# Kernel optimization log

Measured on AMD Instinct MI355X. Metric: run time of the kernel, lower is better.

Reference implementation:

```python
import jax, jax.numpy as jnp
import numpy as np

B, NF, V, D, NI = 16384, 26, 100000, 16, 13
HID = [512, 256, 128, 64, 1]

def setup_inputs() -> dict:
    key = jax.random.key(0)
    ks = jax.random.split(key, 24)
    x_int = jax.random.normal(ks[0], (B, NI), dtype=jnp.float32)
    x_cat = jax.random.randint(ks[1], (B, NF), 0, V, dtype=jnp.int64)
    emb_tables = jax.random.normal(ks[2], (NF, V, D), dtype=jnp.float32) * 0.01
    lin_tables = jax.random.normal(ks[3], (NF, V, 1), dtype=jnp.float32) * 0.01
    W_num = jax.random.normal(ks[4], (NI, 1), dtype=jnp.float32) * 0.1
    b_num = jnp.zeros((1,), dtype=jnp.float32)
    bias = jnp.zeros((1,), dtype=jnp.float32)
    dims = [NF * D + NI] + HID  # 429 -> 512 -> 256 -> 128 -> 64 -> 1
    mlp = {}
    for li in range(5):
        fan_in = dims[li]
        mlp[f'W{li+1}'] = jax.random.normal(ks[5 + 2*li], (dims[li], dims[li+1]), dtype=jnp.float32) / np.sqrt(fan_in)
        mlp[f'b{li+1}'] = jnp.zeros((dims[li+1],), dtype=jnp.float32)
    return dict(x_int=x_int, x_cat=x_cat, emb_tables=emb_tables, lin_tables=lin_tables,
                W_num=W_num, b_num=b_num, bias=bias, **mlp)

def reference(x_int, x_cat, emb_tables, lin_tables, W_num, b_num, bias,
              W1, b1, W2, b2, W3, b3, W4, b4, W5, b5):
    feat_idx = jnp.arange(NF)[None, :]                 # [1, NF]
    emb = emb_tables[feat_idx, x_cat]                  # [B, NF, D] fused gather
    # FM second-order interaction
    sum_emb = jnp.sum(emb, axis=1)                     # [B, D]
    square_of_sum = sum_emb ** 2
    sum_of_square = jnp.sum(emb ** 2, axis=1)
    fm_score = 0.5 * jnp.sum(square_of_sum - sum_of_square, axis=1, keepdims=True)  # [B,1]
    # linear terms
    lin_cat_score = jnp.sum(lin_tables[feat_idx, x_cat], axis=1)  # [B,1]
    lin_num_score = x_int @ W_num + b_num                          # [B,1]
    # deep MLP (dropout is identity at inference)
    deep_in = jnp.concatenate([emb.reshape(emb.shape[0], -1), x_int], axis=1)  # [B, NF*D+NI]
    h = jax.nn.relu(deep_in @ W1 + b1)
    h = jax.nn.relu(h @ W2 + b2)
    h = jax.nn.relu(h @ W3 + b3)
    h = jax.nn.relu(h @ W4 + b4)
    deep_score = h @ W5 + b5                                       # [B,1]
    return bias + lin_cat_score + lin_num_score + fm_score + deep_score
```

## Files before the change

kernel.cpp:

```cpp
#include <hip/hip_runtime.h>
#include <hip/hip_bf16.h>
#include <stdint.h>

typedef __bf16 bf16x8 __attribute__((ext_vector_type(8)));
typedef __bf16 bf16x4 __attribute__((ext_vector_type(4)));
typedef float  f32x4  __attribute__((ext_vector_type(4)));

#define NROWS 16384
#define NFEAT 26
#define VOCAB 100000

__device__ __forceinline__ void bar_lgkm() {
  asm volatile("s_waitcnt lgkmcnt(0)" ::: "memory");
  __builtin_amdgcn_s_barrier();
  asm volatile("" ::: "memory");
}

template<int KPAD, int KREAL, int N, int NCT, int WS>
__device__ __forceinline__ void mlp_layer(const float* __restrict__ W,
                                          const float* __restrict__ bias,
                                          const __bf16* Ain, __bf16* Aout,
                                          int w, int lane) {
  constexpr int LDA = KPAD + 8, LDO = N + 8;
  const int lrow = lane & 15;
  const int kg = (lane >> 4) * 8;

  f32x4 acc[NCT][4];
  #pragma unroll
  for (int j = 0; j < NCT; ++j)
    #pragma unroll
    for (int m = 0; m < 4; ++m)
      #pragma unroll
      for (int i = 0; i < 4; ++i) acc[j][m][i] = 0.f;

  int col[NCT];
  #pragma unroll
  for (int j = 0; j < NCT; ++j) col[j] = (w + j * WS) * 16 + lrow;

  for (int k0 = 0; k0 < KREAL; k0 += 32) {
    bf16x8 af[4];
    #pragma unroll
    for (int m = 0; m < 4; ++m)
      af[m] = *(const bf16x8*)(Ain + (m * 16 + lrow) * LDA + k0 + kg);
    #pragma unroll
    for (int j = 0; j < NCT; ++j) {
      bf16x8 bw;
      #pragma unroll
      for (int i = 0; i < 8; ++i)
        bw[i] = (__bf16)W[(size_t)(k0 + kg + i) * N + col[j]];
      #pragma unroll
      for (int m = 0; m < 4; ++m)
        acc[j][m] = __builtin_amdgcn_mfma_f32_16x16x32_bf16(af[m], bw, acc[j][m], 0, 0, 0);
    }
  }

  const int rbase = (lane >> 4) * 4;
  #pragma unroll
  for (int j = 0; j < NCT; ++j) {
    float bv = bias[col[j]];
    #pragma unroll
    for (int m = 0; m < 4; ++m)
      #pragma unroll
      for (int i = 0; i < 4; ++i) {
        float v = acc[j][m][i] + bv;
        v = fmaxf(v, 0.f);
        Aout[(m * 16 + rbase + i) * LDO + col[j]] = (__bf16)v;
      }
  }
}

__global__ __launch_bounds__(1024) void k_fused(
    const float* __restrict__ x_int,
    const int*   __restrict__ x_cat,
    const float* __restrict__ emb,
    const float* __restrict__ lin,
    const float* __restrict__ W_num,
    const float* __restrict__ b_num,
    const float* __restrict__ bias0,
    const float* __restrict__ W1, const float* __restrict__ b1,
    const float* __restrict__ W2, const float* __restrict__ b2,
    const float* __restrict__ W3, const float* __restrict__ b3,
    const float* __restrict__ W4, const float* __restrict__ b4,
    const float* __restrict__ W5, const float* __restrict__ b5,
    float* __restrict__ out) {
  __shared__ __align__(16) char smem[125184];
  __bf16* A0 = (__bf16*)smem;
  __bf16* A1 = (__bf16*)(smem + 58368);
  int* s_idx = (int*)(smem + 58368);
  float* s_part = (float*)(smem + 124928);

  const int t = threadIdx.x;
  const int row0 = blockIdx.x * 64;
  const int w = t >> 6, lane = t & 63;
  const int lrow = lane & 15, kg = (lane >> 4) * 8;

  for (int i = t; i < 64 * NFEAT; i += 1024) {
    int r = i / NFEAT, f = i - r * NFEAT;
    s_idx[i] = x_cat[(size_t)(row0 + r) * NFEAT + f];
  }
  __syncthreads();

  const int r = t >> 4, d = t & 15;
  const int g = d >> 2, q = d & 3;

  float lin_s = 0.f;
  if (d < 13) {
    lin_s = lin[(size_t)d * VOCAB + s_idx[r * NFEAT + d]]
          + lin[(size_t)(d + 13) * VOCAB + s_idx[r * NFEAT + d + 13]]
          + x_int[(size_t)(row0 + r) * 13 + d] * W_num[d];
  }
  float xv[4] = {0.f, 0.f, 0.f, 0.f};
  if (d >= 8 && d < 12) {
    int base = (d - 8) * 4;
    #pragma unroll
    for (int i = 0; i < 4; ++i)
      if (base + i < 13) xv[i] = x_int[(size_t)(row0 + r) * 13 + base + i];
  }

  f32x4 pf[7];
  #pragma unroll
  for (int c = 0; c < 7; ++c) {
    int fc = 4 * c + g;
    if (fc < NFEAT) {
      int idx = s_idx[r * NFEAT + fc];
      pf[c] = *(const f32x4*)(emb + ((size_t)fc * VOCAB + idx) * 16 + q * 4);
    }
  }

  f32x4 acc[2][4];
  #pragma unroll
  for (int j = 0; j < 2; ++j)
    #pragma unroll
    for (int m = 0; m < 4; ++m)
      #pragma unroll
      for (int i = 0; i < 4; ++i) acc[j][m][i] = 0.f;
  const int colL1[2] = { w * 16 + lrow, (w + 16) * 16 + lrow };

  float fsum[4] = {0.f,0.f,0.f,0.f}, fsq[4] = {0.f,0.f,0.f,0.f};
  #pragma unroll
  for (int c = 0; c < 7; ++c) {
    const int colbase = c * 64 + g * 16 + q * 4;
    if (4 * c + g < NFEAT) {
      bf16x4 pk;
      #pragma unroll
      for (int i = 0; i < 4; ++i) {
        fsum[i] += pf[c][i]; fsq[i] += pf[c][i] * pf[c][i];
        pk[i] = (__bf16)pf[c][i];
      }
      *(bf16x4*)(A0 + r * 456 + colbase) = pk;
    } else {
      bf16x4 pk;
      #pragma unroll
      for (int i = 0; i < 4; ++i) pk[i] = (__bf16)xv[i];
      *(bf16x4*)(A0 + r * 456 + colbase) = pk;
    }
    bar_lgkm();
    #pragma unroll
    for (int ks = 0; ks < 2; ++ks) {
      const int k0 = c * 64 + ks * 32;
      bf16x8 af[4];
      #pragma unroll
      for (int m = 0; m < 4; ++m)
        af[m] = *(const bf16x8*)(A0 + (m * 16 + lrow) * 456 + k0 + kg);
      #pragma unroll
      for (int j = 0; j < 2; ++j) {
        bf16x8 bw;
        #pragma unroll
        for (int i = 0; i < 8; ++i) {
          int k = k0 + kg + i;
          float v;
          if (c < 6) v = W1[(size_t)k * 512 + colL1[j]];
          else       v = (k < 429) ? W1[(size_t)k * 512 + colL1[j]] : 0.f;
          bw[i] = (__bf16)v;
        }
        #pragma unroll
        for (int m = 0; m < 4; ++m)
          acc[j][m] = __builtin_amdgcn_mfma_f32_16x16x32_bf16(af[m], bw, acc[j][m], 0, 0, 0);
      }
    }
  }

  {
    const int rbase = (lane >> 4) * 4;
    #pragma unroll
    for (int j = 0; j < 2; ++j) {
      float bv = b1[colL1[j]];
      #pragma unroll
      for (int m = 0; m < 4; ++m)
        #pragma unroll
        for (int i = 0; i < 4; ++i) {
          float v = acc[j][m][i] + bv;
          v = fmaxf(v, 0.f);
          A1[(m * 16 + rbase + i) * 520 + colL1[j]] = (__bf16)v;
        }
    }
  }

  {
    #pragma unroll
    for (int i = 0; i < 4; ++i) {
      fsum[i] += __shfl_xor(fsum[i], 4); fsq[i] += __shfl_xor(fsq[i], 4);
      fsum[i] += __shfl_xor(fsum[i], 8); fsq[i] += __shfl_xor(fsq[i], 8);
    }
    float fmq = 0.f;
    #pragma unroll
    for (int i = 0; i < 4; ++i) fmq += fsum[i] * fsum[i] - fsq[i];
    fmq += __shfl_xor(fmq, 1);
    fmq += __shfl_xor(fmq, 2);
    float linred = lin_s;
    #pragma unroll
    for (int off = 1; off < 16; off <<= 1) linred += __shfl_xor(linred, off, 16);
    if (d == 0) s_part[r] = 0.5f * fmq + linred + bias0[0] + b_num[0];
  }
  __syncthreads();

  mlp_layer<512, 512, 256, 1, 16>(W2, b2, A1, A0, w, lane);
  __syncthreads();
  if (w < 8) mlp_layer<256, 256, 128, 1, 8>(W3, b3, A0, A1, w, lane);
  __syncthreads();
  if (w < 4) mlp_layer<128, 128, 64, 1, 4>(W4, b4, A1, A0, w, lane);
  __syncthreads();

  {
    const int rr = t >> 4, gg = t & 15;
    float s = 0.f;
    #pragma unroll
    for (int i = 0; i < 4; ++i)
      s += (float)A0[rr * 72 + gg * 4 + i] * W5[gg * 4 + i];
    #pragma unroll
    for (int off = 1; off < 16; off <<= 1) s += __shfl_xor(s, off, 16);
    if (gg == 0) out[row0 + rr] = s + b5[0] + s_part[rr];
  }
}

extern "C" void kernel_launch(void* const* d_in, const int* in_sizes, int n_in,
                              void* d_out, int out_size, void* d_ws, size_t ws_size,
                              hipStream_t stream) {
  const float* x_int = (const float*)d_in[0];
  const int*   x_cat = (const int*)d_in[1];
  const float* emb   = (const float*)d_in[2];
  const float* lin   = (const float*)d_in[3];
  const float* W_num = (const float*)d_in[4];
  const float* b_num = (const float*)d_in[5];
  const float* bias  = (const float*)d_in[6];
  const float* W1 = (const float*)d_in[7];  const float* b1 = (const float*)d_in[8];
  const float* W2 = (const float*)d_in[9];  const float* b2 = (const float*)d_in[10];
  const float* W3 = (const float*)d_in[11]; const float* b3 = (const float*)d_in[12];
  const float* W4 = (const float*)d_in[13]; const float* b4 = (const float*)d_in[14];
  const float* W5 = (const float*)d_in[15]; const float* b5 = (const float*)d_in[16];
  float* out = (float*)d_out;

  k_fused<<<NROWS / 64, 1024, 0, stream>>>(x_int, x_cat, emb, lin, W_num, b_num, bias,
                                           W1, b1, W2, b2, W3, b3, W4, b4, W5, b5,
                                           out);
}
```

Before: 49.66 us.

## Warp-specialize layer 1: producer warps gather embeddings, consumer warps run MFMA

Splits the 16 waves into 8 producer waves and 8 consumer waves. The producers gather embedding rows with a two-chunk-ahead software pipeline and write bf16 activations into shared memory. The consumers run the first-layer MFMAs over four column tiles each, staying in step with the producers through per-chunk barriers. The aim is to overlap the latency of the random embedding gather with the tensor-core work. The cost is that only half the waves issue MFMAs, and each consumer wave holds more accumulator registers.

```diff
diff --git a/kernel.cpp b/kernel.cpp
--- a/kernel.cpp
+++ b/kernel.cpp
@@ -68,6 +68,32 @@
       }
   }
 }
+
+#define P_ISSUE(c)                                                            \
+  if ((c) < 6 || a == 0) {                                                    \
+    int f_ = 4 * (c) + 2 * a;                                                 \
+    int i0_ = s_idx[sbase + f_], i1_ = s_idx[sbase + f_ + 1];                 \
+    pe[(c)][0] = *(const f32x4*)(emb + ((size_t)f_ * VOCAB + i0_) * 16 + q4); \
+    pe[(c)][1] = *(const f32x4*)(emb + ((size_t)(f_ + 1) * VOCAB + i1_) * 16 + q4); \
+  }
+
+#define P_CONSUME(c)                                                          \
+  if ((c) < 6 || a == 0) {                                                    \
+    int f_ = 4 * (c) + 2 * a;                                                 \
+    bf16x4 pk0, pk1;                                                          \
+    for (int i = 0; i < 4; ++i) {                                             \
+      float v0 = pe[(c)][0][i], v1 = pe[(c)][1][i];                           \
+      fsum[i] += v0 + v1; fsq[i] += v0 * v0 + v1 * v1;                        \
+      pk0[i] = (__bf16)v0; pk1[i] = (__bf16)v1;                               \
+    }                                                                         \
+    *(bf16x4*)(A0 + pr * 456 + f_ * 16 + q4) = pk0;                           \
+    *(bf16x4*)(A0 + pr * 456 + (f_ + 1) * 16 + q4) = pk1;                     \
+  } else {                                                                    \
+    bf16x4 pk, pz;                                                            \
+    for (int i = 0; i < 4; ++i) { pk[i] = (__bf16)txv[i]; pz[i] = (__bf16)0.f; } \
+    *(bf16x4*)(A0 + pr * 456 + 416 + q4) = pk;                                \
+    *(bf16x4*)(A0 + pr * 456 + 432 + q4) = pz;                                \
+  }
 
 __global__ __launch_bounds__(1024) void k_fused(
     const float* __restrict__ x_int,
@@ -100,117 +126,106 @@
   }
   __syncthreads();
 
-  const int r = t >> 4, d = t & 15;
-  const int g = d >> 2, q = d & 3;
-
-  float lin_s = 0.f;
-  if (d < 13) {
-    lin_s = lin[(size_t)d * VOCAB + s_idx[r * NFEAT + d]]
-          + lin[(size_t)(d + 13) * VOCAB + s_idx[r * NFEAT + d + 13]]
-          + x_int[(size_t)(row0 + r) * 13 + d] * W_num[d];
-  }
-  float xv[4] = {0.f, 0.f, 0.f, 0.f};
-  if (d >= 8 && d < 12) {
-    int base = (d - 8) * 4;
-    #pragma unroll
-    for (int i = 0; i < 4; ++i)
-      if (base + i < 13) xv[i] = x_int[(size_t)(row0 + r) * 13 + base + i];
-  }
-
-  f32x4 pf[7];
-  #pragma unroll
-  for (int c = 0; c < 7; ++c) {
-    int fc = 4 * c + g;
-    if (fc < NFEAT) {
-      int idx = s_idx[r * NFEAT + fc];
-      pf[c] = *(const f32x4*)(emb + ((size_t)fc * VOCAB + idx) * 16 + q * 4);
-    }
-  }
-
-  f32x4 acc[2][4];
-  #pragma unroll
-  for (int j = 0; j < 2; ++j)
-    #pragma unroll
-    for (int m = 0; m < 4; ++m)
-      #pragma unroll
-      for (int i = 0; i < 4; ++i) acc[j][m][i] = 0.f;
-  const int colL1[2] = { w * 16 + lrow, (w + 16) * 16 + lrow };
-
-  float fsum[4] = {0.f,0.f,0.f,0.f}, fsq[4] = {0.f,0.f,0.f,0.f};
-  #pragma unroll
-  for (int c = 0; c < 7; ++c) {
-    const int colbase = c * 64 + g * 16 + q * 4;
-    if (4 * c + g < NFEAT) {
-      bf16x4 pk;
+  if (w < 8) {
+    const int pid = t;
+    const int pr = pid >> 3;
+    const int sub = pid & 7, a = sub >> 2, q4 = (sub & 3) * 4;
+    const int sbase = pr * NFEAT;
+
+    float lin_acc = lin[(size_t)sub * VOCAB + s_idx[sbase + sub]]
+                  + lin[(size_t)(sub + 8) * VOCAB + s_idx[sbase + sub + 8]]
+                  + lin[(size_t)(sub + 16) * VOCAB + s_idx[sbase + sub + 16]];
+    if (sub < 2)
+      lin_acc += lin[(size_t)(sub + 24) * VOCAB + s_idx[sbase + sub + 24]];
+    float lnum = x_int[(size_t)(row0 + pr) * 13 + sub] * W_num[sub];
+    if (sub < 5)
+      lnum += x_int[(size_t)(row0 + pr) * 13 + sub + 8] * W_num[sub + 8];
+    float txv[4] = {0.f, 0.f, 0.f, 0.f};
+    if (a == 1) {
       #pragma unroll
       for (int i = 0; i < 4; ++i) {
-        fsum[i] += pf[c][i]; fsq[i] += pf[c][i] * pf[c][i];
-        pk[i] = (__bf16)pf[c][i];
+        int ii = q4 + i;
+        if (ii < 13) txv[i] = x_int[(size_t)(row0 + pr) * 13 + ii];
       }
-      *(bf16x4*)(A0 + r * 456 + colbase) = pk;
-    } else {
-      bf16x4 pk;
-      #pragma unroll
-      for (int i = 0; i < 4; ++i) pk[i] = (__bf16)xv[i];
-      *(bf16x4*)(A0 + r * 456 + colbase) = pk;
-    }
-    bar_lgkm();
-    #pragma unroll
-    for (int ks = 0; ks < 2; ++ks) {
-      const int k0 = c * 64 + ks * 32;
-      bf16x8 af[4];
+    }
+
+    float fsum[4] = {0.f,0.f,0.f,0.f}, fsq[4] = {0.f,0.f,0.f,0.f};
+    f32x4 pe[7][2];
+    P_ISSUE(0); P_ISSUE(1);
+    P_ISSUE(2); P_CONSUME(0); bar_lgkm();
+    P_ISSUE(3); P_CONSUME(1); bar_lgkm();
+    P_ISSUE(4); P_CONSUME(2); bar_lgkm();
+    P_ISSUE(5); P_CONSUME(3); bar_lgkm();
+    P_ISSUE(6); P_CONSUME(4); bar_lgkm();
+    P_CONSUME(5); bar_lgkm();
+    P_CONSUME(6); bar_lgkm();
+
+    #pragma unroll
+    for (int i = 0; i < 4; ++i) {
+      fsum[i] += __shfl_xor(fsum[i], 4);
+      fsq[i]  += __shfl_xor(fsq[i], 4);
+    }
+    float fmq = 0.f;
+    #pragma unroll
+    for (int i = 0; i < 4; ++i) fmq += fsum[i] * fsum[i] - fsq[i];
+    fmq += __shfl_xor(fmq, 1);
+    fmq += __shfl_xor(fmq, 2);
+    float lt = lin_acc + lnum;
+    lt += __shfl_xor(lt, 1); lt += __shfl_xor(lt, 2); lt += __shfl_xor(lt, 4);
+    if (sub == 0) s_part[pr] = 0.5f * fmq + lt + bias0[0] + b_num[0];
+  } else {
+    const int cw = w - 8;
+    f32x4 acc[4][4];
+    #pragma unroll
+    for (int j = 0; j < 4; ++j)
       #pragma unroll
       for (int m = 0; m < 4; ++m)
-        af[m] = *(const bf16x8*)(A0 + (m * 16 + lrow) * 456 + k0 + kg);
-      #pragma unroll
-      for (int j = 0; j < 2; ++j) {
-        bf16x8 bw;
-        #pragma unroll
-        for (int i = 0; i < 8; ++i) {
-          int k = k0 + kg + i;
-          float v;
-          if (c < 6) v = W1[(size_t)k * 512 + colL1[j]];
-          else       v = (k < 429) ? W1[(size_t)k * 512 + colL1[j]] : 0.f;
-          bw[i] = (__bf16)v;
+        #pragma unroll
+        for (int i = 0; i < 4; ++i) acc[j][m][i] = 0.f;
+    int col[4];
+    #pragma unroll
+    for (int j = 0; j < 4; ++j) col[j] = (cw + j * 8) * 16 + lrow;
+
+    #pragma unroll
+    for (int c = 0; c < 7; ++c) {
+      bar_lgkm();
+      #pragma unroll
+      for (int ks = 0; ks < 2; ++ks) {
+        const int k0 = c * 64 + ks * 32;
+        bf16x8 af[4];
+        #pragma unroll
+        for (int m = 0; m < 4; ++m)
+          af[m] = *(const bf16x8*)(A0 + (m * 16 + lrow) * 456 + k0 + kg);
+        #pragma unroll
+        for (int j = 0; j < 4; ++j) {
+          bf16x8 bw;
+          #pragma unroll
+          for (int i = 0; i < 8; ++i) {
+            int k = k0 + kg + i;
+            float v;
+            if (c < 6) v = W1[(size_t)k * 512 + col[j]];
+            else       v = (k < 429) ? W1[(size_t)k * 512 + col[j]] : 0.f;
+            bw[i] = (__bf16)v;
+          }
+          #pragma unroll
+          for (int m = 0; m < 4; ++m)
+            acc[j][m] = __builtin_amdgcn_mfma_f32_16x16x32_bf16(af[m], bw, acc[j][m], 0, 0, 0);
         }
-        #pragma unroll
-        for (int m = 0; m < 4; ++m)
-          acc[j][m] = __builtin_amdgcn_mfma_f32_16x16x32_bf16(af[m], bw, acc[j][m], 0, 0, 0);
       }
     }
-  }
-
-  {
     const int rbase = (lane >> 4) * 4;
     #pragma unroll
-    for (int j = 0; j < 2; ++j) {
-      float bv = b1[colL1[j]];
+    for (int j = 0; j < 4; ++j) {
+      float bv = b1[col[j]];
       #pragma unroll
       for (int m = 0; m < 4; ++m)
         #pragma unroll
         for (int i = 0; i < 4; ++i) {
           float v = acc[j][m][i] + bv;
           v = fmaxf(v, 0.f);
-          A1[(m * 16 + rbase + i) * 520 + colL1[j]] = (__bf16)v;
+          A1[(m * 16 + rbase + i) * 520 + col[j]] = (__bf16)v;
         }
     }
-  }
-
-  {
-    #pragma unroll
-    for (int i = 0; i < 4; ++i) {
-      fsum[i] += __shfl_xor(fsum[i], 4); fsq[i] += __shfl_xor(fsq[i], 4);
-      fsum[i] += __shfl_xor(fsum[i], 8); fsq[i] += __shfl_xor(fsq[i], 8);
-    }
-    float fmq = 0.f;
-    #pragma unroll
-    for (int i = 0; i < 4; ++i) fmq += fsum[i] * fsum[i] - fsq[i];
-    fmq += __shfl_xor(fmq, 1);
-    fmq += __shfl_xor(fmq, 2);
-    float linred = lin_s;
-    #pragma unroll
-    for (int off = 1; off < 16; off <<= 1) linred += __shfl_xor(linred, off, 16);
-    if (d == 0) s_part[r] = 0.5f * fmq + linred + bias0[0] + b_num[0];
   }
   __syncthreads();
 
```

New measurement: 73.10 us. 47.2% more time.

## Software-pipeline W1 weight loads and embedding gathers in layer-1 loop

Applied to the files above, without the earlier changes.

Restructures the first MLP layer loop into 14 K-steps, with W1 weight fragments prefetched two steps ahead into a double-buffered register array. Embedding gathers are issued three chunks ahead through a rotating 4-entry buffer instead of all up front. The goal is to overlap global-memory latency for weights and gathered embeddings with the MFMA work. It raises register pressure at 1024 threads per block, which could cause spills.

```diff
diff --git a/kernel.cpp b/kernel.cpp
--- a/kernel.cpp
+++ b/kernel.cpp
@@ -103,6 +103,25 @@
   const int r = t >> 4, d = t & 15;
   const int g = d >> 2, q = d & 3;
 
+  const int colL1[2] = { w * 16 + lrow, (w + 16) * 16 + lrow };
+
+  float wbuf[2][2][8];
+  #pragma unroll
+  for (int sb = 0; sb < 2; ++sb)
+    #pragma unroll
+    for (int j = 0; j < 2; ++j)
+      #pragma unroll
+      for (int i = 0; i < 8; ++i)
+        wbuf[sb][j][i] = W1[(size_t)(sb * 32 + kg + i) * 512 + colL1[j]];
+
+  f32x4 pe[4];
+  #pragma unroll
+  for (int c = 0; c < 3; ++c) {
+    int fc = 4 * c + g;
+    int idx = s_idx[r * NFEAT + fc];
+    pe[c] = *(const f32x4*)(emb + ((size_t)fc * VOCAB + idx) * 16 + q * 4);
+  }
+
   float lin_s = 0.f;
   if (d < 13) {
     lin_s = lin[(size_t)d * VOCAB + s_idx[r * NFEAT + d]]
@@ -117,16 +136,6 @@
       if (base + i < 13) xv[i] = x_int[(size_t)(row0 + r) * 13 + base + i];
   }
 
-  f32x4 pf[7];
-  #pragma unroll
-  for (int c = 0; c < 7; ++c) {
-    int fc = 4 * c + g;
-    if (fc < NFEAT) {
-      int idx = s_idx[r * NFEAT + fc];
-      pf[c] = *(const f32x4*)(emb + ((size_t)fc * VOCAB + idx) * 16 + q * 4);
-    }
-  }
-
   f32x4 acc[2][4];
   #pragma unroll
   for (int j = 0; j < 2; ++j)
@@ -134,50 +143,65 @@
     for (int m = 0; m < 4; ++m)
       #pragma unroll
       for (int i = 0; i < 4; ++i) acc[j][m][i] = 0.f;
-  const int colL1[2] = { w * 16 + lrow, (w + 16) * 16 + lrow };
 
   float fsum[4] = {0.f,0.f,0.f,0.f}, fsq[4] = {0.f,0.f,0.f,0.f};
-  #pragma unroll
-  for (int c = 0; c < 7; ++c) {
-    const int colbase = c * 64 + g * 16 + q * 4;
-    if (4 * c + g < NFEAT) {
-      bf16x4 pk;
-      #pragma unroll
-      for (int i = 0; i < 4; ++i) {
-        fsum[i] += pf[c][i]; fsq[i] += pf[c][i] * pf[c][i];
-        pk[i] = (__bf16)pf[c][i];
+
+  #pragma unroll
+  for (int s = 0; s < 14; ++s) {
+    const int c = s >> 1;
+    bf16x8 bw[2];
+    #pragma unroll
+    for (int j = 0; j < 2; ++j)
+      #pragma unroll
+      for (int i = 0; i < 8; ++i)
+        bw[j][i] = (__bf16)wbuf[s & 1][j][i];
+    if (s + 2 < 14) {
+      #pragma unroll
+      for (int j = 0; j < 2; ++j)
+        #pragma unroll
+        for (int i = 0; i < 8; ++i) {
+          const int k = (s + 2) * 32 + kg + i;
+          float v = 0.f;
+          if (s + 2 < 13 || k < 429)
+            v = W1[(size_t)k * 512 + colL1[j]];
+          wbuf[s & 1][j][i] = v;
+        }
+    }
+    if ((s & 1) == 0) {
+      if (c + 3 <= 6) {
+        const int fc = 4 * (c + 3) + g;
+        if (fc < NFEAT) {
+          int idx = s_idx[r * NFEAT + fc];
+          pe[(c + 3) & 3] = *(const f32x4*)(emb + ((size_t)fc * VOCAB + idx) * 16 + q * 4);
+        }
       }
-      *(bf16x4*)(A0 + r * 456 + colbase) = pk;
-    } else {
-      bf16x4 pk;
-      #pragma unroll
-      for (int i = 0; i < 4; ++i) pk[i] = (__bf16)xv[i];
-      *(bf16x4*)(A0 + r * 456 + colbase) = pk;
-    }
-    bar_lgkm();
-    #pragma unroll
-    for (int ks = 0; ks < 2; ++ks) {
-      const int k0 = c * 64 + ks * 32;
-      bf16x8 af[4];
+      const int colbase = c * 64 + g * 16 + q * 4;
+      if (4 * c + g < NFEAT) {
+        f32x4 cv = pe[c & 3];
+        bf16x4 pk;
+        #pragma unroll
+        for (int i = 0; i < 4; ++i) {
+          fsum[i] += cv[i]; fsq[i] += cv[i] * cv[i];
+          pk[i] = (__bf16)cv[i];
+        }
+        *(bf16x4*)(A0 + r * 456 + colbase) = pk;
+      } else {
+        bf16x4 pk;
+        #pragma unroll
+        for (int i = 0; i < 4; ++i) pk[i] = (__bf16)xv[i];
+        *(bf16x4*)(A0 + r * 456 + colbase) = pk;
+      }
+      bar_lgkm();
+    }
+    bf16x8 af[4];
+    #pragma unroll
+    for (int m = 0; m < 4; ++m)
+      af[m] = *(const bf16x8*)(A0 + (m * 16 + lrow) * 456 + s * 32 + kg);
+    #pragma unroll
+    for (int j = 0; j < 2; ++j)
       #pragma unroll
       for (int m = 0; m < 4; ++m)
-        af[m] = *(const bf16x8*)(A0 + (m * 16 + lrow) * 456 + k0 + kg);
-      #pragma unroll
-      for (int j = 0; j < 2; ++j) {
-        bf16x8 bw;
-        #pragma unroll
-        for (int i = 0; i < 8; ++i) {
-          int k = k0 + kg + i;
-          float v;
-          if (c < 6) v = W1[(size_t)k * 512 + colL1[j]];
-          else       v = (k < 429) ? W1[(size_t)k * 512 + colL1[j]] : 0.f;
-          bw[i] = (__bf16)v;
-        }
-        #pragma unroll
-        for (int m = 0; m < 4; ++m)
-          acc[j][m] = __builtin_amdgcn_mfma_f32_16x16x32_bf16(af[m], bw, acc[j][m], 0, 0, 0);
-      }
-    }
+        acc[j][m] = __builtin_amdgcn_mfma_f32_16x16x32_bf16(af[m], bw[j], acc[j][m], 0, 0, 0);
   }
 
   {
```

After: 63.49 us. 27.8% more time.

## Split fused DeepFM kernel into high-occupancy gather kernel and MLP kernel

Applied to the files above, without the earlier changes.

Moves embedding/linear gathers, FM and linear-term reductions into a separate 512-thread kernel that writes bf16 deep inputs and per-row partial scores to workspace. The MLP kernel then bulk-loads contiguous bf16 activations into LDS and runs layer 1 without per-chunk barriers interleaved with gathers. This aims to hide random gather latency with higher occupancy, at the cost of an extra launch and a workspace round trip of the activation matrix.

```diff
diff --git a/kernel.cpp b/kernel.cpp
--- a/kernel.cpp
+++ b/kernel.cpp
@@ -10,10 +10,80 @@
 #define NFEAT 26
 #define VOCAB 100000
 
-__device__ __forceinline__ void bar_lgkm() {
-  asm volatile("s_waitcnt lgkmcnt(0)" ::: "memory");
-  __builtin_amdgcn_s_barrier();
-  asm volatile("" ::: "memory");
+__global__ __launch_bounds__(512, 8) void k_gather(
+    const float* __restrict__ x_int, const int* __restrict__ x_cat,
+    const float* __restrict__ emb, const float* __restrict__ lin,
+    const float* __restrict__ W_num, const float* __restrict__ b_num,
+    const float* __restrict__ bias0,
+    __bf16* __restrict__ deep_in, float* __restrict__ partial) {
+  __shared__ int s_idx[32 * NFEAT];
+  const int t = threadIdx.x;
+  const int row0 = blockIdx.x * 32;
+  for (int i = t; i < 32 * NFEAT; i += 512) {
+    int r = i / NFEAT, f = i - r * NFEAT;
+    s_idx[i] = x_cat[(size_t)(row0 + r) * NFEAT + f];
+  }
+  __syncthreads();
+
+  const int r = t >> 4, sub = t & 15, h = sub >> 2, q = sub & 3;
+  const int row = row0 + r;
+  const int sbase = r * NFEAT;
+
+  f32x4 pf[7];
+  #pragma unroll
+  for (int j = 0; j < 7; ++j) {
+    int f = 4 * j + h;
+    if (f < NFEAT) {
+      int idx = s_idx[sbase + f];
+      pf[j] = *(const f32x4*)(emb + ((size_t)f * VOCAB + idx) * 16 + q * 4);
+    }
+  }
+
+  float lt = lin[(size_t)sub * VOCAB + s_idx[sbase + sub]];
+  if (sub < 10) lt += lin[(size_t)(sub + 16) * VOCAB + s_idx[sbase + sub + 16]];
+  if (sub < 13) lt += x_int[(size_t)row * 13 + sub] * W_num[sub];
+
+  if (sub < 8) {
+    bf16x4 pk;
+    #pragma unroll
+    for (int i = 0; i < 4; ++i) {
+      int c = sub * 4 + i;
+      float v = (c < 13) ? x_int[(size_t)row * 13 + c] : 0.f;
+      pk[i] = (__bf16)v;
+    }
+    *(bf16x4*)(deep_in + (size_t)row * 448 + 416 + sub * 4) = pk;
+  }
+
+  float fsum[4] = {0.f,0.f,0.f,0.f}, fsq[4] = {0.f,0.f,0.f,0.f};
+  #pragma unroll
+  for (int j = 0; j < 7; ++j) {
+    int f = 4 * j + h;
+    if (f < NFEAT) {
+      bf16x4 pk;
+      #pragma unroll
+      for (int i = 0; i < 4; ++i) {
+        float v = pf[j][i];
+        fsum[i] += v; fsq[i] += v * v;
+        pk[i] = (__bf16)v;
+      }
+      *(bf16x4*)(deep_in + (size_t)row * 448 + f * 16 + q * 4) = pk;
+    }
+  }
+
+  #pragma unroll
+  for (int i = 0; i < 4; ++i) {
+    fsum[i] += __shfl_xor(fsum[i], 4); fsq[i] += __shfl_xor(fsq[i], 4);
+    fsum[i] += __shfl_xor(fsum[i], 8); fsq[i] += __shfl_xor(fsq[i], 8);
+  }
+  float fmq = 0.f;
+  #pragma unroll
+  for (int i = 0; i < 4; ++i) fmq += fsum[i] * fsum[i] - fsq[i];
+  fmq += __shfl_xor(fmq, 1);
+  fmq += __shfl_xor(fmq, 2);
+  lt += __shfl_xor(lt, 1); lt += __shfl_xor(lt, 2);
+  lt += __shfl_xor(lt, 4); lt += __shfl_xor(lt, 8);
+  if (sub == 0)
+    partial[row] = 0.5f * fmq + lt + bias0[0] + b_num[0];
 }
 
 template<int KPAD, int KREAL, int N, int NCT, int WS>
@@ -69,63 +139,31 @@
   }
 }
 
-__global__ __launch_bounds__(1024) void k_fused(
-    const float* __restrict__ x_int,
-    const int*   __restrict__ x_cat,
-    const float* __restrict__ emb,
-    const float* __restrict__ lin,
-    const float* __restrict__ W_num,
-    const float* __restrict__ b_num,
-    const float* __restrict__ bias0,
+__global__ __launch_bounds__(1024, 4) void k_mlp(
+    const __bf16* __restrict__ deep_in, const float* __restrict__ partial,
     const float* __restrict__ W1, const float* __restrict__ b1,
     const float* __restrict__ W2, const float* __restrict__ b2,
     const float* __restrict__ W3, const float* __restrict__ b3,
     const float* __restrict__ W4, const float* __restrict__ b4,
     const float* __restrict__ W5, const float* __restrict__ b5,
     float* __restrict__ out) {
-  __shared__ __align__(16) char smem[125184];
+  __shared__ __align__(16) char smem[124928];
   __bf16* A0 = (__bf16*)smem;
   __bf16* A1 = (__bf16*)(smem + 58368);
-  int* s_idx = (int*)(smem + 58368);
-  float* s_part = (float*)(smem + 124928);
 
   const int t = threadIdx.x;
   const int row0 = blockIdx.x * 64;
   const int w = t >> 6, lane = t & 63;
   const int lrow = lane & 15, kg = (lane >> 4) * 8;
 
-  for (int i = t; i < 64 * NFEAT; i += 1024) {
-    int r = i / NFEAT, f = i - r * NFEAT;
-    s_idx[i] = x_cat[(size_t)(row0 + r) * NFEAT + f];
-  }
-  __syncthreads();
-
-  const int r = t >> 4, d = t & 15;
-  const int g = d >> 2, q = d & 3;
-
-  float lin_s = 0.f;
-  if (d < 13) {
-    lin_s = lin[(size_t)d * VOCAB + s_idx[r * NFEAT + d]]
-          + lin[(size_t)(d + 13) * VOCAB + s_idx[r * NFEAT + d + 13]]
-          + x_int[(size_t)(row0 + r) * 13 + d] * W_num[d];
-  }
-  float xv[4] = {0.f, 0.f, 0.f, 0.f};
-  if (d >= 8 && d < 12) {
-    int base = (d - 8) * 4;
-    #pragma unroll
-    for (int i = 0; i < 4; ++i)
-      if (base + i < 13) xv[i] = x_int[(size_t)(row0 + r) * 13 + base + i];
-  }
-
-  f32x4 pf[7];
-  #pragma unroll
-  for (int c = 0; c < 7; ++c) {
-    int fc = 4 * c + g;
-    if (fc < NFEAT) {
-      int idx = s_idx[r * NFEAT + fc];
-      pf[c] = *(const f32x4*)(emb + ((size_t)fc * VOCAB + idx) * 16 + q * 4);
-    }
-  }
+  {
+    const __bf16* src = deep_in + (size_t)row0 * 448;
+    for (int i = t; i < 3584; i += 1024) {
+      int rr = i / 56, cc = i - rr * 56;
+      *(f32x4*)(A0 + rr * 456 + cc * 8) = *(const f32x4*)(src + (size_t)i * 8);
+    }
+  }
+  __syncthreads();
 
   f32x4 acc[2][4];
   #pragma unroll
@@ -136,47 +174,26 @@
       for (int i = 0; i < 4; ++i) acc[j][m][i] = 0.f;
   const int colL1[2] = { w * 16 + lrow, (w + 16) * 16 + lrow };
 
-  float fsum[4] = {0.f,0.f,0.f,0.f}, fsq[4] = {0.f,0.f,0.f,0.f};
-  #pragma unroll
-  for (int c = 0; c < 7; ++c) {
-    const int colbase = c * 64 + g * 16 + q * 4;
-    if (4 * c + g < NFEAT) {
-      bf16x4 pk;
-      #pragma unroll
-      for (int i = 0; i < 4; ++i) {
-        fsum[i] += pf[c][i]; fsq[i] += pf[c][i] * pf[c][i];
-        pk[i] = (__bf16)pf[c][i];
+  #pragma unroll
+  for (int s = 0; s < 14; ++s) {
+    bf16x8 af[4];
+    #pragma unroll
+    for (int m = 0; m < 4; ++m)
+      af[m] = *(const bf16x8*)(A0 + (m * 16 + lrow) * 456 + s * 32 + kg);
+    #pragma unroll
+    for (int j = 0; j < 2; ++j) {
+      bf16x8 bw;
+      #pragma unroll
+      for (int i = 0; i < 8; ++i) {
+        const int k = s * 32 + kg + i;
+        float v;
+        if (s < 13) v = W1[(size_t)k * 512 + colL1[j]];
+        else        v = (k < 429) ? W1[(size_t)k * 512 + colL1[j]] : 0.f;
+        bw[i] = (__bf16)v;
       }
-      *(bf16x4*)(A0 + r * 456 + colbase) = pk;
-    } else {
-      bf16x4 pk;
-      #pragma unroll
-      for (int i = 0; i < 4; ++i) pk[i] = (__bf16)xv[i];
-      *(bf16x4*)(A0 + r * 456 + colbase) = pk;
-    }
-    bar_lgkm();
-    #pragma unroll
-    for (int ks = 0; ks < 2; ++ks) {
-      const int k0 = c * 64 + ks * 32;
-      bf16x8 af[4];
       #pragma unroll
       for (int m = 0; m < 4; ++m)
-        af[m] = *(const bf16x8*)(A0 + (m * 16 + lrow) * 456 + k0 + kg);
-      #pragma unroll
-      for (int j = 0; j < 2; ++j) {
-        bf16x8 bw;
-        #pragma unroll
-        for (int i = 0; i < 8; ++i) {
-          int k = k0 + kg + i;
-          float v;
-          if (c < 6) v = W1[(size_t)k * 512 + colL1[j]];
-          else       v = (k < 429) ? W1[(size_t)k * 512 + colL1[j]] : 0.f;
-          bw[i] = (__bf16)v;
-        }
-        #pragma unroll
-        for (int m = 0; m < 4; ++m)
-          acc[j][m] = __builtin_amdgcn_mfma_f32_16x16x32_bf16(af[m], bw, acc[j][m], 0, 0, 0);
-      }
+        acc[j][m] = __builtin_amdgcn_mfma_f32_16x16x32_bf16(af[m], bw, acc[j][m], 0, 0, 0);
     }
   }
 
@@ -195,23 +212,6 @@
         }
     }
   }
-
-  {
-    #pragma unroll
-    for (int i = 0; i < 4; ++i) {
-      fsum[i] += __shfl_xor(fsum[i], 4); fsq[i] += __shfl_xor(fsq[i], 4);
-      fsum[i] += __shfl_xor(fsum[i], 8); fsq[i] += __shfl_xor(fsq[i], 8);
-    }
-    float fmq = 0.f;
-    #pragma unroll
-    for (int i = 0; i < 4; ++i) fmq += fsum[i] * fsum[i] - fsq[i];
-    fmq += __shfl_xor(fmq, 1);
-    fmq += __shfl_xor(fmq, 2);
-    float linred = lin_s;
-    #pragma unroll
-    for (int off = 1; off < 16; off <<= 1) linred += __shfl_xor(linred, off, 16);
-    if (d == 0) s_part[r] = 0.5f * fmq + linred + bias0[0] + b_num[0];
-  }
   __syncthreads();
 
   mlp_layer<512, 512, 256, 1, 16>(W2, b2, A1, A0, w, lane);
@@ -229,7 +229,7 @@
       s += (float)A0[rr * 72 + gg * 4 + i] * W5[gg * 4 + i];
     #pragma unroll
     for (int off = 1; off < 16; off <<= 1) s += __shfl_xor(s, off, 16);
-    if (gg == 0) out[row0 + rr] = s + b5[0] + s_part[rr];
+    if (gg == 0) out[row0 + rr] = s + b5[0] + partial[row0 + rr];
   }
 }
 
@@ -250,7 +250,13 @@
   const float* W5 = (const float*)d_in[15]; const float* b5 = (const float*)d_in[16];
   float* out = (float*)d_out;
 
-  k_fused<<<NROWS / 64, 1024, 0, stream>>>(x_int, x_cat, emb, lin, W_num, b_num, bias,
-                                           W1, b1, W2, b2, W3, b3, W4, b4, W5, b5,
-                                           out);
-}
+  char* ws = (char*)d_ws;
+  __bf16* deep_in = (__bf16*)ws;
+  float* partial = (float*)(ws + 14680064);
+
+  k_gather<<<NROWS / 32, 512, 0, stream>>>(x_int, x_cat, emb, lin, W_num, b_num, bias,
+                                           deep_in, partial);
+  k_mlp<<<NROWS / 64, 1024, 0, stream>>>(deep_in, partial,
+                                         W1, b1, W2, b2, W3, b3, W4, b4, W5, b5,
+                                         out);
+}
```

New measurement: 53.64 us. 8.0% more time.
